# Kernel optimization log

Measured on AMD Instinct MI355X. Metric: run time of the kernel, lower is better.

## Reference

```python
import jax, jax.numpy as jnp
import numpy as np

H, W = 128, 128
N_GAUSS = 1024


def _rotmats(q):
    # q: [N,4] (w,x,y,z) -> [N,3,3]
    q = q / jnp.linalg.norm(q, axis=1, keepdims=True)
    w, x, y, z = q[:, 0], q[:, 1], q[:, 2], q[:, 3]
    r0 = jnp.stack([1 - 2 * (y * y + z * z), 2 * (x * y - w * z), 2 * (x * z + w * y)], -1)
    r1 = jnp.stack([2 * (x * y + w * z), 1 - 2 * (x * x + z * z), 2 * (y * z - w * x)], -1)
    r2 = jnp.stack([2 * (x * z - w * y), 2 * (y * z + w * x), 1 - 2 * (x * x + y * y)], -1)
    return jnp.stack([r0, r1, r2], axis=1)


def _project(means_3d, scales, rotations, K):
    fx, fy, cx, cy = K[0, 0], K[1, 1], K[0, 2], K[1, 2]
    X, Y, Z = means_3d[:, 0], means_3d[:, 1], means_3d[:, 2]
    z_inv = 1.0 / (Z + 1e-6)
    means_2d = jnp.stack([fx * X * z_inv + cx, fy * Y * z_inv + cy], axis=1)  # [N,2]
    R = _rotmats(rotations)                      # [N,3,3]
    RS = R * scales[:, None, :]                  # R @ diag(s)
    cov_3d = RS @ jnp.swapaxes(RS, 1, 2)         # [N,3,3]
    zeros = jnp.zeros_like(X)
    j0 = jnp.stack([fx * z_inv, zeros, -fx * X * z_inv * z_inv], -1)
    j1 = jnp.stack([zeros, fy * z_inv, -fy * Y * z_inv * z_inv], -1)
    J = jnp.stack([j0, j1], axis=1)              # [N,2,3]
    cov_2d = J @ cov_3d @ jnp.swapaxes(J, 1, 2) + 1e-4 * jnp.eye(2, dtype=means_3d.dtype)
    return means_2d, cov_2d, Z


def _render(positions, scales, rotations, colors, opacities, K, background):
    means_2d, cov_2d, depths = _project(positions, scales, rotations, K)
    order = jnp.argsort(-depths)  # back-to-front (descending depth)
    m2 = means_2d[order]
    c2 = cov_2d[order]
    col = colors[order]
    op = opacities[order, 0]
    dep = depths[order]

    yy, xx = jnp.meshgrid(jnp.arange(H, dtype=jnp.float32),
                          jnp.arange(W, dtype=jnp.float32), indexing='ij')
    pix = jnp.stack([xx, yy], axis=-1)  # [H,W,2]

    image0 = jnp.broadcast_to(background.astype(jnp.float32), (H, W, 3))
    carry0 = (image0, jnp.zeros((H, W), jnp.float32), jnp.zeros((H, W), jnp.float32))

    def step(carry, g):
        image, depth_map, alpha_acc = carry
        mean, cov, color, opac, depth = g
        in_bounds = ((mean[0] >= -50.0) & (mean[0] <= W + 50.0) &
                     (mean[1] >= -50.0) & (mean[1] <= H + 50.0))
        a, b, c, d = cov[0, 0], cov[0, 1], cov[1, 0], cov[1, 1]
        det = a * d - b * c
        cov_inv = jnp.stack([jnp.stack([d, -b]), jnp.stack([-c, a])]) / det  # [2,2]
        diff = pix - mean  # [H,W,2]
        mahal = jnp.einsum('hwi,ij,hwj->hw', diff, cov_inv, diff)
        weight = jnp.exp(-0.5 * mahal) * opac
        # torch: mask = weight > 0.01, skip gaussian if center far off-screen
        alpha = jnp.where((weight > 0.01) & in_bounds, weight, 0.0)
        contrib = (1.0 - alpha_acc) * alpha  # front-to-back transmittance blend
        image = image + contrib[..., None] * color
        depth_map = depth_map + contrib * depth
        alpha_acc = alpha_acc + contrib
        return (image, depth_map, alpha_acc), None

    (image, depth_map, alpha_acc), _ = jax.lax.scan(step, carry0, (m2, c2, col, op, dep))
    return jnp.clip(image, 0.0, 1.0), depth_map, alpha_acc


def setup_inputs() -> dict:
    key = jax.random.key(0)
    k1, k2, k3, k4, k5, k6 = jax.random.split(key, 6)
    xy = jax.random.normal(k1, (N_GAUSS, 2), jnp.float32)            # spread over view
    z = 3.0 + 5.0 * jax.random.uniform(k2, (N_GAUSS, 1), jnp.float32)  # z in [3, 8]
    positions = jnp.concatenate([xy, z], axis=1)
    scales = 0.01 + 0.10 * jax.random.uniform(k3, (N_GAUSS, 3), jnp.float32)
    rotations = jax.random.normal(k4, (N_GAUSS, 4), jnp.float32)
    colors = jax.random.uniform(k5, (N_GAUSS, 3), jnp.float32)
    opacities = jax.random.uniform(k6, (N_GAUSS, 1), jnp.float32)
    K = jnp.array([[150.0, 0.0, W / 2.0], [0.0, 150.0, H / 2.0], [0.0, 0.0, 1.0]], jnp.float32)
    background = jnp.zeros(3, jnp.float32)
    return {"positions": positions, "scales": scales, "rotations": rotations,
            "colors": colors, "opacities": opacities, "K": K, "background": background}


def reference(positions, scales, rotations, colors, opacities, K, background):
    image, depth_map, alpha_acc = _render(positions, scales, rotations, colors,
                                          opacities, K, background)
    return image, depth_map, alpha_acc
```

## Files before the change

kernel.cpp:

```cpp
#include <hip/hip_runtime.h>
#include <hip/hip_fp16.h>
#include <math.h>


#define NG 1024
#define WID 128
#define HEI 128

__global__ __launch_bounds__(256) void splat_k(
    const float* __restrict__ pos, const float* __restrict__ scl,
    const float* __restrict__ rot, const float* __restrict__ col,
    const float* __restrict__ opa, const float* __restrict__ Km,
    const float* __restrict__ bg, float* __restrict__ out)
{
    __shared__ __align__(16) float4 recA[NG];
    __shared__ __align__(16) float4 recB[NG];
    __shared__ __align__(16) float4 cullL[NG];
    __shared__ __align__(16) float sdep[NG + 4];
    __shared__ int list[NG];
    __shared__ int slist2[NG];
    __shared__ unsigned long long masks[16];
    __shared__ int counts[16];

    int tid = threadIdx.x;
    float fx = Km[0], fy = Km[4], cx = Km[2], cy = Km[5];

    #pragma unroll
    for (int k = 0; k < 4; ++k) {
        int g = k * 256 + tid;

        float X = pos[g*3+0], Y = pos[g*3+1], Z = pos[g*3+2];
        float sx = scl[g*3+0], sy = scl[g*3+1], sz = scl[g*3+2];
        float qw = rot[g*4+0], qx = rot[g*4+1], qy = rot[g*4+2], qz = rot[g*4+3];

        float qn = 1.0f / sqrtf(qw*qw + qx*qx + qy*qy + qz*qz);
        qw *= qn; qx *= qn; qy *= qn; qz *= qn;

        float r00 = 1.f - 2.f*(qy*qy + qz*qz), r01 = 2.f*(qx*qy - qw*qz), r02 = 2.f*(qx*qz + qw*qy);
        float r10 = 2.f*(qx*qy + qw*qz), r11 = 1.f - 2.f*(qx*qx + qz*qz), r12 = 2.f*(qy*qz - qw*qx);
        float r20 = 2.f*(qx*qz - qw*qy), r21 = 2.f*(qy*qz + qw*qx), r22 = 1.f - 2.f*(qx*qx + qy*qy);

        float m00 = r00*sx, m01 = r01*sy, m02 = r02*sz;
        float m10 = r10*sx, m11 = r11*sy, m12 = r12*sz;
        float m20 = r20*sx, m21 = r21*sy, m22 = r22*sz;

        float c00 = m00*m00 + m01*m01 + m02*m02;
        float c01 = m00*m10 + m01*m11 + m02*m12;
        float c02 = m00*m20 + m01*m21 + m02*m22;
        float c11 = m10*m10 + m11*m11 + m12*m12;
        float c12 = m10*m20 + m11*m21 + m12*m22;
        float c22 = m20*m20 + m21*m21 + m22*m22;

        float zinv = 1.0f / (Z + 1e-6f);
        float mx = fx * X * zinv + cx;
        float my = fy * Y * zinv + cy;

        float j00 = fx * zinv,  j02 = -fx * X * zinv * zinv;
        float j11 = fy * zinv,  j12 = -fy * Y * zinv * zinv;

        float a0 = j00*c00 + j02*c02;
        float a1 = j00*c01 + j02*c12;
        float a2 = j00*c02 + j02*c22;
        float b1 = j11*c11 + j12*c12;
        float b2 = j11*c12 + j12*c22;

        float va = a0*j00 + a2*j02 + 1e-4f;
        float vb = a1*j11 + a2*j12;
        float vd = b1*j11 + b2*j12 + 1e-4f;

        float det  = va*vd - vb*vb;
        float idet = 1.0f / det;

        const float kf = -0.5f * 1.44269504088896340736f;
        float ias = kf * vd * idet;
        float ibs = -2.0f * kf * vb * idet;
        float ids = kf * va * idet;

        bool inb = (mx >= -50.f) && (mx <= (float)(WID + 50)) &&
                   (my >= -50.f) && (my <= (float)(HEI + 50));
        float op = inb ? opa[g] : 0.f;

        float lmax = 0.5f*(va + vd) + sqrtf(0.25f*(va - vd)*(va - vd) + vb*vb);
        float R2 = -1.0f;
        if (op > 0.01f) {
            float mthr = 2.0f * (__logf(op) + 4.6051701859880914f);
            R2 = lmax * mthr * 1.02f + 0.01f;
        }

        union { __half2 h2; float f; } urg, ubo;
        urg.h2 = __floats2half2_rn(col[g*3+0], col[g*3+1]);
        ubo.h2 = __floats2half2_rn(col[g*3+2], op);

        recA[g]  = make_float4(mx, my, ias, ibs);
        recB[g]  = make_float4(ids, Z, urg.f, ubo.f);
        cullL[g] = make_float4(mx, my, R2, 0.f);
    }
    __syncthreads();

    int wv = tid >> 6, ln = tid & 63;
    int bx = blockIdx.x & 15, by = blockIdx.x >> 4;
    float x0 = (float)(bx*8), x1 = x0 + 7.f;
    float y0 = (float)(by*8), y1 = y0 + 7.f;

    #pragma unroll
    for (int r = 0; r < 4; ++r) {
        int gr = wv*4 + r;
        float4 c = cullL[gr*64 + ln];
        float ddx = fmaxf(fmaxf(x0 - c.x, c.x - x1), 0.f);
        float ddy = fmaxf(fmaxf(y0 - c.y, c.y - y1), 0.f);
        bool keep = (ddx*ddx + ddy*ddy) < c.z;
        unsigned long long m = __ballot(keep);
        if (ln == 0) { masks[gr] = m; counts[gr] = (int)__popcll(m); }
    }
    __syncthreads();

    int len = 0;
    #pragma unroll
    for (int j = 0; j < 16; ++j) len += counts[j];

    #pragma unroll
    for (int r = 0; r < 4; ++r) {
        int gr = wv*4 + r;
        int base = 0;
        #pragma unroll
        for (int j = 0; j < 16; ++j) base += (j < gr) ? counts[j] : 0;
        unsigned long long m = masks[gr];
        if ((m >> ln) & 1ull) {
            int id = gr*64 + ln;
            int p = base + (int)__popcll(m & ((1ull << ln) - 1ull));
            list[p] = id;
            sdep[p] = recB[id].y;
        }
    }
    if (tid < 4) sdep[len + tid] = -INFINITY;
    __syncthreads();

    const float4* sdep4 = (const float4*)sdep;
    int L4r = (len + 3) >> 2;
    for (int i = tid; i < len; i += 256) {
        float d = sdep[i];
        int rank = 0;
        for (int j4 = 0; j4 < L4r; ++j4) {
            float4 z = sdep4[j4];
            int jb = j4*4;
            rank += (z.x > d || (z.x == d && (jb+0) < i)) ? 1 : 0;
            rank += (z.y > d || (z.y == d && (jb+1) < i)) ? 1 : 0;
            rank += (z.z > d || (z.z == d && (jb+2) < i)) ? 1 : 0;
            rank += (z.w > d || (z.w == d && (jb+3) < i)) ? 1 : 0;
        }
        slist2[rank] = list[i];
    }
    __syncthreads();

    int p   = tid & 3;
    int pix = tid >> 2;
    int px  = bx*8 + (pix & 7);
    int py  = by*8 + (pix >> 3);
    float fpx = (float)px, fpy = (float)py;

    int L4 = (len + 3) >> 2;
    int s0 = p * L4;
    int s1 = min(len, s0 + L4);

    float T = 1.f, sr = 0.f, sg = 0.f, sb = 0.f, sd = 0.f, sa = 0.f;
    for (int i = s0; i < s1; ++i) {
        int id = slist2[i];
        float4 f0 = recA[id];
        float4 f1 = recB[id];

        float mx = f0.x, my = f0.y, ias = f0.z, ibs = f0.w;
        float ids = f1.x, dep = f1.y;
        union { float f; __half2 h2; } urg, ubo;
        urg.f = f1.z; ubo.f = f1.w;
        float cr = __low2float(urg.h2), cg = __high2float(urg.h2);
        float cb = __low2float(ubo.h2), op = __high2float(ubo.h2);

        float dx = fpx - mx, dy = fpy - my;
        float arg = ias*(dx*dx) + ibs*(dx*dy) + ids*(dy*dy);
        float w = exp2f(arg) * op;
        float al = (w > 0.01f) ? w : 0.f;
        float c = T * al;
        sr = fmaf(c, cr, sr);
        sg = fmaf(c, cg, sg);
        sb = fmaf(c, cb, sb);
        sd = fmaf(c, dep, sd);
        sa += c;
        T  -= c;
    }

    float v = T;
    #pragma unroll
    for (int d = 1; d < 4; d <<= 1) {
        float u = __shfl_up(v, d, 4);
        if (p >= d) v *= u;
    }
    float pre = __shfl_up(v, 1, 4);
    float P = (p == 0) ? 1.f : pre;

    sr *= P; sg *= P; sb *= P; sd *= P; sa *= P;
    #pragma unroll
    for (int m = 1; m < 4; m <<= 1) {
        sr += __shfl_xor(sr, m, 4);
        sg += __shfl_xor(sg, m, 4);
        sb += __shfl_xor(sb, m, 4);
        sd += __shfl_xor(sd, m, 4);
        sa += __shfl_xor(sa, m, 4);
    }

    if (p == 0) {
        int idx = py * WID + px;
        out[idx*3+0] = fminf(fmaxf(bg[0] + sr, 0.f), 1.f);
        out[idx*3+1] = fminf(fmaxf(bg[1] + sg, 0.f), 1.f);
        out[idx*3+2] = fminf(fmaxf(bg[2] + sb, 0.f), 1.f);
        out[HEI*WID*3 + idx] = sd;
        out[HEI*WID*4 + idx] = sa;
    }
}

extern "C" void kernel_launch(void* const* d_in, const int* in_sizes, int n_in,
                              void* d_out, int out_size, void* d_ws, size_t ws_size,
                              hipStream_t stream)
{
    const float* pos = (const float*)d_in[0];
    const float* scl = (const float*)d_in[1];
    const float* rot = (const float*)d_in[2];
    const float* col = (const float*)d_in[3];
    const float* opa = (const float*)d_in[4];
    const float* Km  = (const float*)d_in[5];
    const float* bg  = (const float*)d_in[6];
    float* out = (float*)d_out;

    hipLaunchKernelGGL(splat_k, dim3(256), dim3(256), 0, stream,
                       pos, scl, rot, col, opa, Km, bg, out);
}
```

Before: 16.48 us.

## Use 1024-thread blocks: one gaussian per thread, 16-way split per pixel

Raises the block size from 256 to 1024 threads. Each thread now preprocesses a single gaussian, and each pixel's depth-sorted list is split across 16 lanes instead of 4, with the transmittance scan and reductions widened to 16 lanes. The cull pass reuses recA for the means and keeps only a compact R2 array, and the rotation quaternion is read as one float4. The aim is to shorten the serial per-thread loops in preprocessing, sorting and compositing. The cost is more shuffle steps, fewer registers per thread, and at most one 1024-thread block resident per CU given the shared memory use.

After: 14.16 us. 14.1% less time.

```diff
diff --git a/kernel.cpp b/kernel.cpp
--- a/kernel.cpp
+++ b/kernel.cpp
@@ -7,7 +7,7 @@
 #define WID 128
 #define HEI 128
 
-__global__ __launch_bounds__(256) void splat_k(
+__global__ __launch_bounds__(1024) void splat_k(
     const float* __restrict__ pos, const float* __restrict__ scl,
     const float* __restrict__ rot, const float* __restrict__ col,
     const float* __restrict__ opa, const float* __restrict__ Km,
@@ -15,7 +15,7 @@
 {
     __shared__ __align__(16) float4 recA[NG];
     __shared__ __align__(16) float4 recB[NG];
-    __shared__ __align__(16) float4 cullL[NG];
+    __shared__ float cullR2[NG];
     __shared__ __align__(16) float sdep[NG + 4];
     __shared__ int list[NG];
     __shared__ int slist2[NG];
@@ -23,15 +23,15 @@
     __shared__ int counts[16];
 
     int tid = threadIdx.x;
+    int wv = tid >> 6, ln = tid & 63;
     float fx = Km[0], fy = Km[4], cx = Km[2], cy = Km[5];
 
-    #pragma unroll
-    for (int k = 0; k < 4; ++k) {
-        int g = k * 256 + tid;
-
+    {
+        int g = tid;
         float X = pos[g*3+0], Y = pos[g*3+1], Z = pos[g*3+2];
         float sx = scl[g*3+0], sy = scl[g*3+1], sz = scl[g*3+2];
-        float qw = rot[g*4+0], qx = rot[g*4+1], qy = rot[g*4+2], qz = rot[g*4+3];
+        float4 q4 = ((const float4*)rot)[g];
+        float qw = q4.x, qx = q4.y, qy = q4.z, qz = q4.w;
 
         float qn = 1.0f / sqrtf(qw*qw + qx*qx + qy*qy + qz*qz);
         qw *= qn; qx *= qn; qy *= qn; qz *= qn;
@@ -91,55 +91,49 @@
         urg.h2 = __floats2half2_rn(col[g*3+0], col[g*3+1]);
         ubo.h2 = __floats2half2_rn(col[g*3+2], op);
 
-        recA[g]  = make_float4(mx, my, ias, ibs);
-        recB[g]  = make_float4(ids, Z, urg.f, ubo.f);
-        cullL[g] = make_float4(mx, my, R2, 0.f);
-    }
-    __syncthreads();
-
-    int wv = tid >> 6, ln = tid & 63;
+        recA[g]   = make_float4(mx, my, ias, ibs);
+        recB[g]   = make_float4(ids, Z, urg.f, ubo.f);
+        cullR2[g] = R2;
+    }
+    __syncthreads();
+
     int bx = blockIdx.x & 15, by = blockIdx.x >> 4;
     float x0 = (float)(bx*8), x1 = x0 + 7.f;
     float y0 = (float)(by*8), y1 = y0 + 7.f;
-
-    #pragma unroll
-    for (int r = 0; r < 4; ++r) {
-        int gr = wv*4 + r;
-        float4 c = cullL[gr*64 + ln];
-        float ddx = fmaxf(fmaxf(x0 - c.x, c.x - x1), 0.f);
-        float ddy = fmaxf(fmaxf(y0 - c.y, c.y - y1), 0.f);
-        bool keep = (ddx*ddx + ddy*ddy) < c.z;
+    {
+        float4 a = recA[tid];
+        float R2 = cullR2[tid];
+        float ddx = fmaxf(fmaxf(x0 - a.x, a.x - x1), 0.f);
+        float ddy = fmaxf(fmaxf(y0 - a.y, a.y - y1), 0.f);
+        bool keep = (ddx*ddx + ddy*ddy) < R2;
         unsigned long long m = __ballot(keep);
-        if (ln == 0) { masks[gr] = m; counts[gr] = (int)__popcll(m); }
+        if (ln == 0) { masks[wv] = m; counts[wv] = (int)__popcll(m); }
     }
     __syncthreads();
 
     int len = 0;
     #pragma unroll
     for (int j = 0; j < 16; ++j) len += counts[j];
-
-    #pragma unroll
-    for (int r = 0; r < 4; ++r) {
-        int gr = wv*4 + r;
+    {
         int base = 0;
         #pragma unroll
-        for (int j = 0; j < 16; ++j) base += (j < gr) ? counts[j] : 0;
-        unsigned long long m = masks[gr];
+        for (int j = 0; j < 16; ++j) base += (j < wv) ? counts[j] : 0;
+        unsigned long long m = masks[wv];
         if ((m >> ln) & 1ull) {
-            int id = gr*64 + ln;
             int p = base + (int)__popcll(m & ((1ull << ln) - 1ull));
-            list[p] = id;
-            sdep[p] = recB[id].y;
+            list[p] = tid;
+            sdep[p] = recB[tid].y;
         }
     }
     if (tid < 4) sdep[len + tid] = -INFINITY;
     __syncthreads();
 
-    const float4* sdep4 = (const float4*)sdep;
-    int L4r = (len + 3) >> 2;
-    for (int i = tid; i < len; i += 256) {
+    if (tid < len) {
+        int i = tid;
         float d = sdep[i];
         int rank = 0;
+        const float4* sdep4 = (const float4*)sdep;
+        int L4r = (len + 3) >> 2;
         for (int j4 = 0; j4 < L4r; ++j4) {
             float4 z = sdep4[j4];
             int jb = j4*4;
@@ -152,15 +146,15 @@
     }
     __syncthreads();
 
-    int p   = tid & 3;
-    int pix = tid >> 2;
+    int p   = tid & 15;
+    int pix = tid >> 4;
     int px  = bx*8 + (pix & 7);
     int py  = by*8 + (pix >> 3);
     float fpx = (float)px, fpy = (float)py;
 
-    int L4 = (len + 3) >> 2;
-    int s0 = p * L4;
-    int s1 = min(len, s0 + L4);
+    int L16 = (len + 15) >> 4;
+    int s0 = p * L16;
+    int s1 = min(len, s0 + L16);
 
     float T = 1.f, sr = 0.f, sg = 0.f, sb = 0.f, sd = 0.f, sa = 0.f;
     for (int i = s0; i < s1; ++i) {
@@ -190,21 +184,21 @@
 
     float v = T;
     #pragma unroll
-    for (int d = 1; d < 4; d <<= 1) {
-        float u = __shfl_up(v, d, 4);
+    for (int d = 1; d < 16; d <<= 1) {
+        float u = __shfl_up(v, d, 16);
         if (p >= d) v *= u;
     }
-    float pre = __shfl_up(v, 1, 4);
+    float pre = __shfl_up(v, 1, 16);
     float P = (p == 0) ? 1.f : pre;
 
     sr *= P; sg *= P; sb *= P; sd *= P; sa *= P;
     #pragma unroll
-    for (int m = 1; m < 4; m <<= 1) {
-        sr += __shfl_xor(sr, m, 4);
-        sg += __shfl_xor(sg, m, 4);
-        sb += __shfl_xor(sb, m, 4);
-        sd += __shfl_xor(sd, m, 4);
-        sa += __shfl_xor(sa, m, 4);
+    for (int m = 1; m < 16; m <<= 1) {
+        sr += __shfl_xor(sr, m, 16);
+        sg += __shfl_xor(sg, m, 16);
+        sb += __shfl_xor(sb, m, 16);
+        sd += __shfl_xor(sd, m, 16);
+        sa += __shfl_xor(sa, m, 16);
     }
 
     if (p == 0) {
@@ -230,6 +224,6 @@
     const float* bg  = (const float*)d_in[6];
     float* out = (float*)d_out;
 
-    hipLaunchKernelGGL(splat_k, dim3(256), dim3(256), 0, stream,
+    hipLaunchKernelGGL(splat_k, dim3(256), dim3(1024), 0, stream,
                        pos, scl, rot, col, opa, Km, bg, out);
 }
```
